# Optimization experiments

Measured on AMD Instinct MI355X. Metric: run time of the kernel, lower is better.

The kernel has to match this reference:

```python
import jax, jax.numpy as jnp
import numpy as np

D_MODEL, D_FF, NUM_EXPERTS, RANK, TOP_K = 1024, 4096, 8, 16, 2
B, S = 8, 2048


def _expert_ffn(h, wi_w, wo_w, A, Bm):
    # h: [B,S,D]; wi_w: [F,D]; wo_w: [D,F]; A: [R,D]; Bm: [F,R]
    inter = jnp.einsum('bsd,fd->bsf', h, wi_w)
    lora = jnp.einsum('bsr,fr->bsf', jnp.einsum('bsd,rd->bsr', h, A), Bm)
    inter = jax.nn.relu(inter + lora)
    return jnp.einsum('bsf,df->bsd', inter, wo_w)


def setup_inputs() -> dict:
    key = jax.random.key(0)
    ks = jax.random.split(key, 8)
    hidden_states = jax.random.normal(ks[0], (B, S, D_MODEL), dtype=jnp.float32)
    wi_w = jax.random.normal(ks[1], (D_FF, D_MODEL), dtype=jnp.float32) * (1.0 / np.sqrt(D_MODEL))
    wo_w = jax.random.normal(ks[2], (D_MODEL, D_FF), dtype=jnp.float32) * (1.0 / np.sqrt(D_FF))
    # kaiming-uniform-ish A; B random (zeros in init, randomized for a meaningful kernel baseline)
    lora_As = jax.random.uniform(ks[3], (NUM_EXPERTS, RANK, D_MODEL), dtype=jnp.float32, minval=-1.0, maxval=1.0) / np.sqrt(D_MODEL)
    lora_Bs = jax.random.normal(ks[4], (NUM_EXPERTS, D_FF, RANK), dtype=jnp.float32) * 0.02
    top_k_indices = jnp.arange(TOP_K, dtype=jnp.int32)  # task-level selected experts, shape [top_k]
    top_k_values = jax.random.uniform(ks[5], (TOP_K,), dtype=jnp.float32)
    return {'hidden_states': hidden_states, 'wi_w': wi_w, 'wo_w': wo_w,
            'lora_As': lora_As, 'lora_Bs': lora_Bs,
            'top_k_indices': top_k_indices, 'top_k_values': top_k_values}


def reference(hidden_states, wi_w, wo_w, lora_As, lora_Bs, top_k_indices, top_k_values):
    # Task-level top-k: each selected expert runs a full LoRA-augmented FFN over
    # all tokens, scaled by its scalar mixed routing weight, then summed.
    # sum_k v_k * ffn_{idx_k}(h) == sum_i (sum_{k: idx_k=i} v_k) * ffn_i(h)  (matches torch loop)
    out = jnp.zeros_like(hidden_states)
    for k in range(top_k_values.shape[0]):
        A = jnp.take(lora_As, top_k_indices[k], axis=0)
        Bm = jnp.take(lora_Bs, top_k_indices[k], axis=0)
        out = out + top_k_values[k] * _expert_ffn(hidden_states, wi_w, wo_w, A, Bm)
    return out
```

## Files before the change

kernel.cpp:

```cpp
#include <hip/hip_runtime.h>
#include <hip/hip_bf16.h>
#include <cstdint>
#include <cstddef>

#define D_MODEL 1024
#define D_FF    4096
#define RANK    16
#define NTOK    16384

typedef __attribute__((ext_vector_type(8))) __bf16 bf16x8;
typedef __attribute__((ext_vector_type(4))) float  f32x4;

using gas_t = const __attribute__((address_space(1))) void*;
using las_t = __attribute__((address_space(3))) void*;

__device__ __forceinline__ unsigned short f2bf(float f) {
    unsigned int u = __builtin_bit_cast(unsigned int, f);
    u += 0x7fffu + ((u >> 16) & 1u);
    return (unsigned short)(u >> 16);
}

__device__ __forceinline__ void gload_lds16(const unsigned short* g, unsigned short* l) {
    __builtin_amdgcn_global_load_lds((gas_t)g, (las_t)l, 16, 0, 0);
}

__global__ void cast_kernel(const float* __restrict__ in, unsigned short* __restrict__ out, int n4) {
    int i = blockIdx.x * blockDim.x + threadIdx.x;
    int stride = gridDim.x * blockDim.x;
    for (; i < n4; i += stride) {
        float4 v = reinterpret_cast<const float4*>(in)[i];
        ushort4 o;
        o.x = f2bf(v.x); o.y = f2bf(v.y); o.z = f2bf(v.z); o.w = f2bf(v.w);
        reinterpret_cast<ushort4*>(out)[i] = o;
    }
}

__global__ void lora_t_kernel(const float* __restrict__ h, const float* __restrict__ As,
                              const int* __restrict__ idx, unsigned short* __restrict__ tcat,
                              unsigned short* __restrict__ hbf) {
    const int m = blockIdx.x;
    const int l = threadIdx.x;
    float hreg[16];
    #pragma unroll
    for (int j = 0; j < 16; ++j) hreg[j] = h[(size_t)m * D_MODEL + j * 64 + l];
    #pragma unroll
    for (int j = 0; j < 16; ++j) hbf[(size_t)m * D_MODEL + j * 64 + l] = f2bf(hreg[j]);
    #pragma unroll
    for (int e = 0; e < 2; ++e) {
        const float* A = As + (size_t)idx[e] * RANK * D_MODEL;
        for (int r = 0; r < RANK; ++r) {
            float s = 0.f;
            #pragma unroll
            for (int j = 0; j < 16; ++j) s += hreg[j] * A[r * D_MODEL + j * 64 + l];
            #pragma unroll
            for (int off = 32; off >= 1; off >>= 1) s += __shfl_xor(s, off, 64);
            if (l == 0) tcat[(size_t)m * 32 + e * 16 + r] = f2bf(s);
        }
    }
}

__global__ void bcat_kernel(const float* __restrict__ Bs, const int* __restrict__ idx,
                            unsigned short* __restrict__ bcat) {
    int i = blockIdx.x * blockDim.x + threadIdx.x;
    if (i >= D_FF * 32) return;
    int f = i >> 5, kk = i & 31;
    int e = kk >> 4, r = kk & 15;
    bcat[i] = f2bf(Bs[(size_t)idx[e] * D_FF * RANK + (size_t)f * RANK + r]);
}

template<int KDIM, int EPI, int OSTRIDE, int GN>
__launch_bounds__(512, 2)
__global__ void gemm256(const unsigned short* __restrict__ A,
                        const unsigned short* __restrict__ Bm,
                        float* __restrict__ outF,
                        unsigned short* __restrict__ outBf,
                        const unsigned short* __restrict__ tcat,
                        const unsigned short* __restrict__ bcat,
                        const float* __restrict__ topv) {
    __shared__ unsigned short lds[2][2][2][128 * 64];
    const int tid  = threadIdx.x;
    const int lane = tid & 63;
    const int wid  = tid >> 6;
    const int wr   = wid >> 2;
    const int wc   = wid & 3;
    const int lr   = lane & 15;
    const int hi   = lane >> 4;
    const int swz  = (lane & 7) << 3;

    const int nwg  = gridDim.x;
    const int orig = blockIdx.x;
    const int wg   = (orig & 7) * (nwg >> 3) + (orig >> 3);
    const int bm0  = (wg / GN) * 256;
    const int bn0  = (wg % GN) * 256;

    constexpr int NKT = KDIM / 64;
    constexpr int NT2 = NKT / 2;

    f32x4 acc[8][4] = {};
    bf16x8 aF[8], b0[4], b1[4];

    auto stage = [&](int buf, int mat, int half, const unsigned short* src, int kt) {
        const int row0 = (mat == 0 ? bm0 : bn0) + half * 128;
        const int k0 = kt * 64;
        #pragma unroll
        for (int p = 0; p < 2; ++p) {
            const int L = p * 8192 + tid * 16;
            const int r = L >> 7;
            const int c = (L & 127) >> 1;
            const int gc = k0 + (c ^ ((r & 7) << 3));
            gload_lds16(src + (size_t)(row0 + r) * KDIM + gc,
                        &lds[buf][mat][half][0] + (L >> 1));
        }
    };
    auto readA = [&](int buf, int qm) {
        #pragma unroll
        for (int fr = 0; fr < 4; ++fr)
            #pragma unroll
            for (int ks = 0; ks < 2; ++ks)
                aF[fr * 2 + ks] = *reinterpret_cast<const bf16x8*>(
                    &lds[buf][0][wr][(qm * 64 + fr * 16 + lr) * 64 + ((ks * 32 + hi * 8) ^ swz)]);
    };
    auto readB = [&](int buf, int qn, bf16x8* bb) {
        #pragma unroll
        for (int fc = 0; fc < 2; ++fc)
            #pragma unroll
            for (int ks = 0; ks < 2; ++ks)
                bb[fc * 2 + ks] = *reinterpret_cast<const bf16x8*>(
                    &lds[buf][1][wc >> 1][((wc & 1) * 64 + qn * 32 + fc * 16 + lr) * 64
                                          + ((ks * 32 + hi * 8) ^ swz)]);
    };
    auto mfma16 = [&](int qm, int qn, const bf16x8* bb) {
        #pragma unroll
        for (int fr = 0; fr < 4; ++fr)
            #pragma unroll
            for (int fc = 0; fc < 2; ++fc)
                #pragma unroll
                for (int ks = 0; ks < 2; ++ks)
                    acc[qm * 4 + fr][qn * 2 + fc] = __builtin_amdgcn_mfma_f32_16x16x32_bf16(
                        aF[fr * 2 + ks], bb[fc * 2 + ks], acc[qm * 4 + fr][qn * 2 + fc], 0, 0, 0);
    };

#define BAR() __builtin_amdgcn_s_barrier()
#define WAIT_LGKM() do { asm volatile("s_waitcnt lgkmcnt(0)" ::: "memory"); \
                         __builtin_amdgcn_sched_barrier(0); } while (0)
#define WAIT_VM(n) do { asm volatile("s_waitcnt vmcnt(" #n ")" ::: "memory"); \
                        __builtin_amdgcn_sched_barrier(0); } while (0)
#define PRIO_MFMA(qm, qn, bb) do { __builtin_amdgcn_s_setprio(1); mfma16(qm, qn, bb); \
                                   __builtin_amdgcn_s_setprio(0); } while (0)

    stage(0, 0, 0, A, 0);  stage(0, 0, 1, A, 0);
    stage(0, 1, 0, Bm, 0); stage(0, 1, 1, Bm, 0);
    stage(1, 1, 0, Bm, 1); stage(1, 1, 1, Bm, 1);
    WAIT_VM(4);
    BAR();

    #pragma unroll 1
    for (int it = 0; it < NT2; ++it) {
        const int t1 = 2 * it + 1;
        const int t2 = (2 * it + 2 < NKT) ? 2 * it + 2 : NKT - 1;
        const int t3 = (2 * it + 3 < NKT) ? 2 * it + 3 : NKT - 1;
        readA(0, 0); readB(0, 0, b0);
        stage(1, 0, 0, A, t1);
        BAR(); WAIT_LGKM(); PRIO_MFMA(0, 0, b0); BAR();
        readB(0, 1, b1);
        stage(1, 0, 1, A, t1);
        BAR(); WAIT_LGKM(); PRIO_MFMA(0, 1, b1); BAR();
        readA(0, 1);
        stage(0, 1, 0, Bm, t2);
        BAR(); WAIT_LGKM(); PRIO_MFMA(1, 0, b0); BAR();
        stage(0, 1, 1, Bm, t2);
        BAR(); PRIO_MFMA(1, 1, b1); WAIT_VM(4); BAR();
        readA(1, 0); readB(1, 0, b0);
        stage(0, 0, 0, A, t2);
        BAR(); WAIT_LGKM(); PRIO_MFMA(0, 0, b0); BAR();
        readB(1, 1, b1);
        stage(0, 0, 1, A, t2);
        BAR(); WAIT_LGKM(); PRIO_MFMA(0, 1, b1); BAR();
        readA(1, 1);
        stage(1, 1, 0, Bm, t3);
        BAR(); WAIT_LGKM(); PRIO_MFMA(1, 0, b0); BAR();
        stage(1, 1, 1, Bm, t3);
        BAR(); PRIO_MFMA(1, 1, b1); WAIT_VM(4); BAR();
    }
    asm volatile("s_waitcnt vmcnt(0)" ::: "memory");
    __builtin_amdgcn_sched_barrier(0);
    BAR();

    const int rbase = bm0 + wr * 128 + hi * 4;
    const int cbase = bn0 + wc * 64 + lr;

    if constexpr (EPI == 1) {
        const float v0 = topv[0], v1 = topv[1];
        const bf16x8 z8 = {};
        bf16x8 bl0[4], bl1[4];
        #pragma unroll
        for (int ni = 0; ni < 4; ++ni) {
            const int f = cbase + ni * 16;
            bf16x8 bfull = *reinterpret_cast<const bf16x8*>(&bcat[(size_t)f * 32 + hi * 8]);
            bl0[ni] = (hi < 2) ? bfull : z8;
            bl1[ni] = (hi < 2) ? z8 : bfull;
        }
        #pragma unroll
        for (int mi = 0; mi < 8; ++mi) {
            const int mrow = bm0 + wr * 128 + mi * 16 + lr;
            const bf16x8 alo = *reinterpret_cast<const bf16x8*>(&tcat[(size_t)mrow * 32 + hi * 8]);
            #pragma unroll
            for (int ni = 0; ni < 4; ++ni) {
                const f32x4 zz = {};
                f32x4 l0 = __builtin_amdgcn_mfma_f32_16x16x32_bf16(alo, bl0[ni], zz, 0, 0, 0);
                f32x4 l1 = __builtin_amdgcn_mfma_f32_16x16x32_bf16(alo, bl1[ni], zz, 0, 0, 0);
                #pragma unroll
                for (int j = 0; j < 4; ++j) {
                    float z = acc[mi][ni][j];
                    float c = v0 * fmaxf(z + l0[j], 0.f) + v1 * fmaxf(z + l1[j], 0.f);
                    outBf[(size_t)(rbase + mi * 16 + j) * OSTRIDE + cbase + ni * 16] = f2bf(c);
                }
            }
        }
    } else {
        #pragma unroll
        for (int mi = 0; mi < 8; ++mi)
            #pragma unroll
            for (int ni = 0; ni < 4; ++ni)
                #pragma unroll
                for (int j = 0; j < 4; ++j)
                    outF[(size_t)(rbase + mi * 16 + j) * OSTRIDE + cbase + ni * 16] = acc[mi][ni][j];
    }
#undef BAR
#undef WAIT_LGKM
#undef WAIT_VM
#undef PRIO_MFMA
}

extern "C" void kernel_launch(void* const* d_in, const int* in_sizes, int n_in,
                              void* d_out, int out_size, void* d_ws, size_t ws_size,
                              hipStream_t stream) {
    const float* h    = (const float*)d_in[0];
    const float* wi   = (const float*)d_in[1];
    const float* wo   = (const float*)d_in[2];
    const float* As   = (const float*)d_in[3];
    const float* Bs   = (const float*)d_in[4];
    const int*   idx  = (const int*)d_in[5];
    const float* topv = (const float*)d_in[6];
    float* out = (float*)d_out;

    char* ws = (char*)d_ws;
    unsigned short* hbf  = (unsigned short*)(ws);
    unsigned short* wibf = (unsigned short*)(ws + 33554432);
    unsigned short* wobf = (unsigned short*)(ws + 41943040);
    unsigned short* tcat = (unsigned short*)(ws + 50331648);
    unsigned short* bcat = (unsigned short*)(ws + 51380224);
    unsigned short* comb = (unsigned short*)(ws + 51642368);

    lora_t_kernel<<<NTOK, 64, 0, stream>>>(h, As, idx, tcat, hbf);
    cast_kernel<<<1024, 256, 0, stream>>>(wi, wibf, (D_FF * D_MODEL) / 4);
    cast_kernel<<<1024, 256, 0, stream>>>(wo, wobf, (D_MODEL * D_FF) / 4);
    bcat_kernel<<<(D_FF * 32) / 256, 256, 0, stream>>>(Bs, idx, bcat);

    gemm256<D_MODEL, 1, D_FF, 16><<<dim3(64 * 16), 512, 0, stream>>>(
        hbf, wibf, nullptr, comb, tcat, bcat, topv);
    gemm256<D_FF, 0, D_MODEL, 4><<<dim3(64 * 4), 512, 0, stream>>>(
        comb, wobf, out, nullptr, nullptr, nullptr, nullptr);
}
```

Before: 348.2 us.

## Compute LoRA down-projection with bf16 MFMA and merge A/B prep into one kernel

Replaces the per-token scalar LoRA down-projection, which ran one wave per token with shuffle reductions over 32 ranks, with an MFMA-based kernel. Each wave handles 16 tokens against a pre-cast bf16 concatenated A matrix while also writing the bf16 copy of the hidden states. A new prep kernel builds both the bf16 concatenated A and B matrices, replacing the separate bcat kernel. The LoRA intermediate is now computed from bf16-rounded hidden states and A weights instead of fp32, which slightly changes numerics.

```diff
diff --git a/kernel.cpp b/kernel.cpp
--- a/kernel.cpp
+++ b/kernel.cpp
@@ -35,37 +35,48 @@
     }
 }
 
-__global__ void lora_t_kernel(const float* __restrict__ h, const float* __restrict__ As,
-                              const int* __restrict__ idx, unsigned short* __restrict__ tcat,
-                              unsigned short* __restrict__ hbf) {
-    const int m = blockIdx.x;
-    const int l = threadIdx.x;
-    float hreg[16];
+__global__ void prep_kernel(const float* __restrict__ Bs, const float* __restrict__ As,
+                            const int* __restrict__ idx,
+                            unsigned short* __restrict__ bcat, unsigned short* __restrict__ acatg) {
+    int i = blockIdx.x * blockDim.x + threadIdx.x;
+    if (i < D_FF * 32) {
+        int f = i >> 5, kk = i & 31, e = kk >> 4, r = kk & 15;
+        bcat[i] = f2bf(Bs[(size_t)idx[e] * D_FF * RANK + (size_t)f * RANK + r]);
+    } else {
+        int j = i - D_FF * 32;
+        int row = j >> 10, col = j & 1023, e = row >> 4, r = row & 15;
+        acatg[j] = f2bf(As[(size_t)idx[e] * RANK * D_MODEL + r * D_MODEL + col]);
+    }
+}
+
+__global__ void lora_t_v2(const float* __restrict__ h,
+                          const unsigned short* __restrict__ acatg,
+                          unsigned short* __restrict__ tcat,
+                          unsigned short* __restrict__ hbf) {
+    const int tid = threadIdx.x, lane = tid & 63, w = tid >> 6;
+    const int tok0 = blockIdx.x * 64 + w * 16;
+    const int lr = lane & 15, kc = lane >> 4;
+    f32x4 acc0 = {}, acc1 = {};
+    const size_t rowoff = (size_t)(tok0 + lr) * D_MODEL;
+    #pragma unroll 4
+    for (int kt = 0; kt < 32; ++kt) {
+        const int k0 = kt * 32 + kc * 8;
+        float4 u0 = *reinterpret_cast<const float4*>(h + rowoff + k0);
+        float4 u1 = *reinterpret_cast<const float4*>(h + rowoff + k0 + 4);
+        union { bf16x8 v; unsigned short s[8]; } af;
+        af.s[0] = f2bf(u0.x); af.s[1] = f2bf(u0.y); af.s[2] = f2bf(u0.z); af.s[3] = f2bf(u0.w);
+        af.s[4] = f2bf(u1.x); af.s[5] = f2bf(u1.y); af.s[6] = f2bf(u1.z); af.s[7] = f2bf(u1.w);
+        *reinterpret_cast<bf16x8*>(&hbf[rowoff + k0]) = af.v;
+        bf16x8 b0 = *reinterpret_cast<const bf16x8*>(&acatg[(size_t)lr * D_MODEL + k0]);
+        bf16x8 b1 = *reinterpret_cast<const bf16x8*>(&acatg[(size_t)(16 + lr) * D_MODEL + k0]);
+        acc0 = __builtin_amdgcn_mfma_f32_16x16x32_bf16(af.v, b0, acc0, 0, 0, 0);
+        acc1 = __builtin_amdgcn_mfma_f32_16x16x32_bf16(af.v, b1, acc1, 0, 0, 0);
+    }
     #pragma unroll
-    for (int j = 0; j < 16; ++j) hreg[j] = h[(size_t)m * D_MODEL + j * 64 + l];
-    #pragma unroll
-    for (int j = 0; j < 16; ++j) hbf[(size_t)m * D_MODEL + j * 64 + l] = f2bf(hreg[j]);
-    #pragma unroll
-    for (int e = 0; e < 2; ++e) {
-        const float* A = As + (size_t)idx[e] * RANK * D_MODEL;
-        for (int r = 0; r < RANK; ++r) {
-            float s = 0.f;
-            #pragma unroll
-            for (int j = 0; j < 16; ++j) s += hreg[j] * A[r * D_MODEL + j * 64 + l];
-            #pragma unroll
-            for (int off = 32; off >= 1; off >>= 1) s += __shfl_xor(s, off, 64);
-            if (l == 0) tcat[(size_t)m * 32 + e * 16 + r] = f2bf(s);
-        }
-    }
-}
-
-__global__ void bcat_kernel(const float* __restrict__ Bs, const int* __restrict__ idx,
-                            unsigned short* __restrict__ bcat) {
-    int i = blockIdx.x * blockDim.x + threadIdx.x;
-    if (i >= D_FF * 32) return;
-    int f = i >> 5, kk = i & 31;
-    int e = kk >> 4, r = kk & 15;
-    bcat[i] = f2bf(Bs[(size_t)idx[e] * D_FF * RANK + (size_t)f * RANK + r]);
+    for (int j = 0; j < 4; ++j) {
+        tcat[(size_t)(tok0 + kc * 4 + j) * 32 + lr]      = f2bf(acc0[j]);
+        tcat[(size_t)(tok0 + kc * 4 + j) * 32 + 16 + lr] = f2bf(acc1[j]);
+    }
 }
 
 template<int KDIM, int EPI, int OSTRIDE, int GN>
@@ -245,17 +256,18 @@
     float* out = (float*)d_out;
 
     char* ws = (char*)d_ws;
-    unsigned short* hbf  = (unsigned short*)(ws);
-    unsigned short* wibf = (unsigned short*)(ws + 33554432);
-    unsigned short* wobf = (unsigned short*)(ws + 41943040);
-    unsigned short* tcat = (unsigned short*)(ws + 50331648);
-    unsigned short* bcat = (unsigned short*)(ws + 51380224);
-    unsigned short* comb = (unsigned short*)(ws + 51642368);
-
-    lora_t_kernel<<<NTOK, 64, 0, stream>>>(h, As, idx, tcat, hbf);
+    unsigned short* hbf   = (unsigned short*)(ws);
+    unsigned short* wibf  = (unsigned short*)(ws + 33554432);
+    unsigned short* wobf  = (unsigned short*)(ws + 41943040);
+    unsigned short* tcat  = (unsigned short*)(ws + 50331648);
+    unsigned short* bcat  = (unsigned short*)(ws + 51380224);
+    unsigned short* acatg = (unsigned short*)(ws + 51642368);
+    unsigned short* comb  = (unsigned short*)(ws + 51707904);
+
+    prep_kernel<<<640, 256, 0, stream>>>(Bs, As, idx, bcat, acatg);
+    lora_t_v2<<<NTOK / 64, 256, 0, stream>>>(h, acatg, tcat, hbf);
     cast_kernel<<<1024, 256, 0, stream>>>(wi, wibf, (D_FF * D_MODEL) / 4);
     cast_kernel<<<1024, 256, 0, stream>>>(wo, wobf, (D_MODEL * D_FF) / 4);
-    bcat_kernel<<<(D_FF * 32) / 256, 256, 0, stream>>>(Bs, idx, bcat);
 
     gemm256<D_MODEL, 1, D_FF, 16><<<dim3(64 * 16), 512, 0, stream>>>(
         hbf, wibf, nullptr, comb, tcat, bcat, topv);
```

New measurement: 289.6 us. -16.8%, faster.
